# Optimization experiments

Measured on AMD Instinct MI355X. Metric: run time of the kernel, lower is better.

## Reference

```python
import jax, jax.numpy as jnp
import numpy as np

B, N, CZ, D = 1, 1024, 128, 6
LN_EPS = 1e-5
MASK_VALUE = 1000000.0  # float32 path in the original


def setup_inputs() -> dict:
    key = jax.random.key(0)
    k1, k2 = jax.random.split(key)
    pair = jax.random.normal(k1, (B, N, N, CZ), dtype=jnp.float32)
    seq_index = jnp.broadcast_to(jnp.arange(N, dtype=jnp.int64), (B, N))
    ln_scale = jnp.ones((CZ,), dtype=jnp.float32)
    ln_bias = jnp.zeros((CZ,), dtype=jnp.float32)
    W = jax.random.normal(k2, (CZ, D), dtype=jnp.float32) * (1.0 / np.sqrt(CZ))
    b = jnp.zeros((D,), dtype=jnp.float32)
    return {"pair": pair, "seq_index": seq_index, "ln_scale": ln_scale,
            "ln_bias": ln_bias, "W": W, "b": b}


def reference(pair, seq_index, ln_scale, ln_bias, W, b):
    # LayerNorm over channel dim
    mu = jnp.mean(pair, axis=-1, keepdims=True)
    var = jnp.mean(jnp.square(pair - mu), axis=-1, keepdims=True)
    h = (pair - mu) * jax.lax.rsqrt(var + LN_EPS) * ln_scale + ln_bias
    # Linear -> [B, N, N, D]
    x = jnp.einsum('bijc,cd->bijd', h, W) + b
    # symmetrize over (i, j)
    x = (x + jnp.swapaxes(x, -3, -2)) * 0.5
    # sequence-separation mask: |i - j| > 3
    si = seq_index[..., :, None]
    sj = seq_index[..., None, :]
    m = jnp.abs(si - sj) > 3  # [B, N, N]
    x = jnp.where(m[..., None], x, -MASK_VALUE)
    # padded triple log_softmax: row (axis -2), column (axis -3), channel (axis -1)
    l = x.shape[-2]
    u = jnp.zeros(x.shape[:-3] + (l, 1, D), dtype=x.dtype)
    v = jnp.zeros(x.shape[:-3] + (1, l, D), dtype=x.dtype)
    w = jnp.zeros(x.shape[:-3] + (l, l, 1), dtype=x.dtype)
    row = jax.nn.log_softmax(jnp.concatenate((u, x), axis=-2), axis=-2)[..., 1:, :]
    col = jax.nn.log_softmax(jnp.concatenate((v, x), axis=-3), axis=-3)[..., 1:, :, :]
    chn = jax.nn.log_softmax(jnp.concatenate((w, x), axis=-1), axis=-1)[..., 1:]
    return row + col + 2.0 * chn
```

## Files before the change

### kernel.cpp

```cpp
#include <hip/hip_runtime.h>

#define NN 1024
#define NP (NN * NN)
#define NBLK 1024
#define NGRP (NBLK * 16)

typedef float f32x4 __attribute__((ext_vector_type(4)));

__device__ __forceinline__ f32x4 ntld(const float* p) {
  return __builtin_nontemporal_load((const f32x4*)p);
}

__device__ __forceinline__ ushort bfr(float f) {
  uint u = __float_as_uint(f);
  return (ushort)((u + 0x7fffu + ((u >> 16) & 1u)) >> 16);
}
__device__ __forceinline__ float ubf(uint u) {
  return __uint_as_float(u << 16);
}

#define DPP_ADD_STAGE(v, ctrl)                                               \
  {                                                                          \
    const int _t = __builtin_amdgcn_update_dpp(                              \
        0, __float_as_int(v), (ctrl), 0xf, 0xf, true);                       \
    (v) += __int_as_float(_t);                                               \
  }

__global__ __launch_bounds__(256) void k_ln_gemv(
    const float* __restrict__ pairp, const float* __restrict__ gamma,
    const float* __restrict__ beta, const float* __restrict__ W,
    const float* __restrict__ bvec, ushort* __restrict__ xout,
    float* __restrict__ rowsum)
{
  if (blockIdx.x == 0) {
    for (int k = threadIdx.x; k < NN * 6; k += 256) rowsum[k] = 0.f;
  }

  const int l = threadIdx.x & 15;
  const int group = blockIdx.x * 16 + (threadIdx.x >> 4);

  float ug[8][6], apart[6] = {0, 0, 0, 0, 0, 0}, bpart[6] = {0, 0, 0, 0, 0, 0};
#pragma unroll
  for (int k = 0; k < 2; ++k)
#pragma unroll
    for (int m = 0; m < 4; ++m) {
      const int c = 4 * l + 64 * k + m;
      const int idx = 4 * k + m;
      const float ga = gamma[c], be = beta[c];
#pragma unroll
      for (int d = 0; d < 6; ++d) {
        const float w = W[c * 6 + d];
        ug[idx][d] = ga * w;
        apart[d] += ga * w;
        bpart[d] += be * w;
      }
    }
#pragma unroll
  for (int d = 0; d < 6; ++d)
#pragma unroll
    for (int m = 1; m <= 8; m <<= 1) {
      apart[d] += __shfl_xor(apart[d], m);
      bpart[d] += __shfl_xor(bpart[d], m);
    }
  const float vA = (l == 0) ? apart[0] : (l == 1) ? apart[1] : (l == 2) ? apart[2]
                  : (l == 3) ? apart[3] : (l == 4) ? apart[4] : apart[5];
  float vB = (l == 0) ? bpart[0] : (l == 1) ? bpart[1] : (l == 2) ? bpart[2]
            : (l == 3) ? bpart[3] : (l == 4) ? bpart[4] : bpart[5];
  if (l < 6) vB += bvec[l];

  size_t p = 2 * (size_t)group;
  const float* bp = pairp + p * 128 + 4 * l;
  f32x4 a0 = ntld(bp), b0 = ntld(bp + 64);
  f32x4 a1 = ntld(bp + 128), b1 = ntld(bp + 192);

  for (int it = 0; it < 32; ++it) {
    const size_t pn = p + 2 * NGRP;
    f32x4 na0, nb0, na1, nb1;
    if (it != 31) {
      const float* nbp = pairp + pn * 128 + 4 * l;
      na0 = ntld(nbp); nb0 = ntld(nbp + 64);
      na1 = ntld(nbp + 128); nb1 = ntld(nbp + 192);
    }

    const float xv0[8] = {a0.x, a0.y, a0.z, a0.w, b0.x, b0.y, b0.z, b0.w};
    const float xv1[8] = {a1.x, a1.y, a1.z, a1.w, b1.x, b1.y, b1.z, b1.w};
    float r[16];
#pragma unroll
    for (int k = 0; k < 16; ++k) r[k] = 0.f;
#pragma unroll
    for (int k = 0; k < 8; ++k) {
      r[0] += xv0[k];
      r[1] = fmaf(xv0[k], xv0[k], r[1]);
      r[8] += xv1[k];
      r[9] = fmaf(xv1[k], xv1[k], r[9]);
#pragma unroll
      for (int d = 0; d < 6; ++d) {
        r[2 + d] = fmaf(xv0[k], ug[k][d], r[2 + d]);
        r[10 + d] = fmaf(xv1[k], ug[k][d], r[10 + d]);
      }
    }
#pragma unroll
    for (int k = 0; k < 16; ++k) DPP_ADD_STAGE(r[k], 0xB1);
#pragma unroll
    for (int k = 0; k < 16; ++k) DPP_ADD_STAGE(r[k], 0x4E);
#pragma unroll
    for (int k = 0; k < 16; ++k) DPP_ADD_STAGE(r[k], 0x141);
#pragma unroll
    for (int k = 0; k < 16; ++k) DPP_ADD_STAGE(r[k], 0x140);

    if (l < 6) {
      const float mu0 = r[0] * (1.f / 128.f);
      const float var0 = r[1] * (1.f / 128.f) - mu0 * mu0;
      const float rstd0 = rsqrtf(var0 + 1e-5f);
      const float vg0 = (l == 0) ? r[2] : (l == 1) ? r[3] : (l == 2) ? r[4]
                       : (l == 3) ? r[5] : (l == 4) ? r[6] : r[7];
      xout[p * 6 + l] = bfr(fmaf(rstd0, vg0 - mu0 * vA, vB));

      const float mu1 = r[8] * (1.f / 128.f);
      const float var1 = r[9] * (1.f / 128.f) - mu1 * mu1;
      const float rstd1 = rsqrtf(var1 + 1e-5f);
      const float vg1 = (l == 0) ? r[10] : (l == 1) ? r[11] : (l == 2) ? r[12]
                       : (l == 3) ? r[13] : (l == 4) ? r[14] : r[15];
      xout[(p + 1) * 6 + l] = bfr(fmaf(rstd1, vg1 - mu1 * vA, vB));
    }
    p = pn;
    a0 = na0; b0 = nb0; a1 = na1; b1 = nb1;
  }
}

__device__ __forceinline__ void do_tile(
    const float* __restrict__ Mr, const float* __restrict__ Mc,
    int rowBand, int colBand, const int* __restrict__ seq,
    ushort* __restrict__ t, float* __restrict__ rowsum, int tid)
{
  float es[4][6];
#pragma unroll
  for (int q = 0; q < 4; ++q) {
    const int e = tid + 256 * q;
    const int r = e >> 5, c = e & 31;
    const int i = rowBand + r, j = colBand + c;
    const int dd = seq[i] - seq[j];
    const bool far = (dd > 3) || (dd < -3);
    const float* mr = &Mr[r * 193 + c * 6];
    const float* mc = &Mc[c * 193 + r * 6];
    float xs[6], chs = 0.f;
#pragma unroll
    for (int d = 0; d < 6; ++d) {
      xs[d] = far ? 0.5f * (mr[d] + mc[d]) : -1000000.f;
      es[q][d] = __expf(xs[d]);
      chs += es[q][d];
    }
    const float c2 = 2.f * logf(1.f + chs);
    uint w0 = (uint)bfr(4.f * xs[0] - c2) | ((uint)bfr(4.f * xs[1] - c2) << 16);
    uint w1 = (uint)bfr(4.f * xs[2] - c2) | ((uint)bfr(4.f * xs[3] - c2) << 16);
    uint w2 = (uint)bfr(4.f * xs[4] - c2) | ((uint)bfr(4.f * xs[5] - c2) << 16);
    uint* tp = (uint*)(t + ((size_t)i * NN + j) * 6);
    tp[0] = w0; tp[1] = w1; tp[2] = w2;
  }
#pragma unroll
  for (int q = 0; q < 4; ++q)
#pragma unroll
    for (int d = 0; d < 6; ++d)
#pragma unroll
      for (int m = 1; m <= 16; m <<= 1) es[q][d] += __shfl_xor(es[q][d], m);
  if ((tid & 31) == 0) {
    const int w = tid >> 5;
#pragma unroll
    for (int q = 0; q < 4; ++q) {
      const int i = rowBand + w + 8 * q;
#pragma unroll
      for (int d = 0; d < 6; ++d) atomicAdd(&rowsum[i * 6 + d], es[q][d]);
    }
  }
}

__global__ __launch_bounds__(256) void k_sym2(
    const ushort* __restrict__ x, const int* __restrict__ seq,
    ushort* __restrict__ t, float* __restrict__ rowsum)
{
  const int b = blockIdx.x;
  int I = (int)((sqrtf(8.f * b + 1.f) - 1.f) * 0.5f);
  while ((I + 1) * (I + 2) / 2 <= b) ++I;
  while (I * (I + 1) / 2 > b) --I;
  const int J = b - I * (I + 1) / 2;
  const int tid = threadIdx.x;

  __shared__ float M1[32 * 193];
  __shared__ float M2[32 * 193];

  for (int k = tid; k < 768; k += 256) {
    const int m = k / 24, f = (k % 24) * 8;
    {
      const uint4 raw = *(const uint4*)(x + ((size_t)(I * 32 + m) * NN + J * 32) * 6 + f);
      float* dst = &M1[m * 193 + f];
      dst[0] = ubf(raw.x & 0xffff); dst[1] = ubf(raw.x >> 16);
      dst[2] = ubf(raw.y & 0xffff); dst[3] = ubf(raw.y >> 16);
      dst[4] = ubf(raw.z & 0xffff); dst[5] = ubf(raw.z >> 16);
      dst[6] = ubf(raw.w & 0xffff); dst[7] = ubf(raw.w >> 16);
    }
    if (I != J) {
      const uint4 raw = *(const uint4*)(x + ((size_t)(J * 32 + m) * NN + I * 32) * 6 + f);
      float* dst = &M2[m * 193 + f];
      dst[0] = ubf(raw.x & 0xffff); dst[1] = ubf(raw.x >> 16);
      dst[2] = ubf(raw.y & 0xffff); dst[3] = ubf(raw.y >> 16);
      dst[4] = ubf(raw.z & 0xffff); dst[5] = ubf(raw.z >> 16);
      dst[6] = ubf(raw.w & 0xffff); dst[7] = ubf(raw.w >> 16);
    }
  }
  __syncthreads();

  if (I != J) {
    do_tile(M1, M2, I * 32, J * 32, seq, t, rowsum, tid);
    do_tile(M2, M1, J * 32, I * 32, seq, t, rowsum, tid);
  } else {
    do_tile(M1, M1, I * 32, J * 32, seq, t, rowsum, tid);
  }
}

__global__ __launch_bounds__(256) void k_out2(
    const ushort* __restrict__ t, const float* __restrict__ rowsum,
    float* __restrict__ out)
{
  const int b = blockIdx.x;
  const int i = b >> 2;
  const int j = ((b & 3) << 8) + threadIdx.x;

  __shared__ float LSI[6];
  if (threadIdx.x < 6) LSI[threadIdx.x] = logf(1.f + rowsum[i * 6 + threadIdx.x]);
  __syncthreads();

  float lj[6];
#pragma unroll
  for (int d = 0; d < 6; ++d) lj[d] = logf(1.f + rowsum[j * 6 + d]);

  const size_t p = (size_t)i * NN + j;
  const uint* tp = (const uint*)(t + p * 6);
  const uint w0 = tp[0], w1 = tp[1], w2 = tp[2];
  float o[6];
  o[0] = ubf(w0 & 0xffff) - LSI[0] - lj[0];
  o[1] = ubf(w0 >> 16)    - LSI[1] - lj[1];
  o[2] = ubf(w1 & 0xffff) - LSI[2] - lj[2];
  o[3] = ubf(w1 >> 16)    - LSI[3] - lj[3];
  o[4] = ubf(w2 & 0xffff) - LSI[4] - lj[4];
  o[5] = ubf(w2 >> 16)    - LSI[5] - lj[5];

  float* op = out + p * 6;
  *(float2*)(op) = make_float2(o[0], o[1]);
  *(float2*)(op + 2) = make_float2(o[2], o[3]);
  *(float2*)(op + 4) = make_float2(o[4], o[5]);
}

extern "C" void kernel_launch(void* const* d_in, const int* in_sizes, int n_in,
                              void* d_out, int out_size, void* d_ws, size_t ws_size,
                              hipStream_t stream) {
  const float* pairp = (const float*)d_in[0];
  const int* seq = (const int*)d_in[1];
  const float* gamma = (const float*)d_in[2];
  const float* beta = (const float*)d_in[3];
  const float* W = (const float*)d_in[4];
  const float* bvec = (const float*)d_in[5];
  float* out = (float*)d_out;

  ushort* x = (ushort*)d_ws;
  ushort* t = x + (size_t)NP * 6;
  float* rowsum = (float*)(t + (size_t)NP * 6);

  k_ln_gemv<<<NBLK, 256, 0, stream>>>(pairp, gamma, beta, W, bvec, x, rowsum);
  k_sym2<<<528, 256, 0, stream>>>(x, seq, t, rowsum);
  k_out2<<<NP / 256, 256, 0, stream>>>(t, rowsum, out);
}
```

Measured before the change: 133.5 us.

## Fuse symmetrize and output kernels with a grid-wide barrier, dropping t intermediate

Merges the symmetrize/softmax tile kernel and the final output kernel into one kernel. Each block first accumulates its exp row sums with atomics, then all blocks meet at a grid-wide barrier built on an atomic counter, and each block finishes by writing the final fp32 output directly from its shared-memory tiles. This removes the bf16 t intermediate write and read-back and one kernel launch, at the cost of recomputing exp values. It also relies on all 528 blocks being co-resident so the spin barrier cannot deadlock.

```diff
diff --git a/kernel.cpp b/kernel.cpp
--- a/kernel.cpp
+++ b/kernel.cpp
@@ -4,6 +4,7 @@
 #define NP (NN * NN)
 #define NBLK 1024
 #define NGRP (NBLK * 16)
+#define NTRI 528
 
 typedef float f32x4 __attribute__((ext_vector_type(4)));
 
@@ -30,10 +31,11 @@
     const float* __restrict__ pairp, const float* __restrict__ gamma,
     const float* __restrict__ beta, const float* __restrict__ W,
     const float* __restrict__ bvec, ushort* __restrict__ xout,
-    float* __restrict__ rowsum)
+    float* __restrict__ rowsum, int* __restrict__ done)
 {
   if (blockIdx.x == 0) {
     for (int k = threadIdx.x; k < NN * 6; k += 256) rowsum[k] = 0.f;
+    if (threadIdx.x == 0) *done = 0;
   }
 
   const int l = threadIdx.x & 15;
@@ -128,12 +130,46 @@
   }
 }
 
-__device__ __forceinline__ void do_tile(
-    const float* __restrict__ Mr, const float* __restrict__ Mc,
-    int rowBand, int colBand, const int* __restrict__ seq,
-    ushort* __restrict__ t, float* __restrict__ rowsum, int tid)
+__device__ __forceinline__ void phaseA(
+    const float* __restrict__ Mr, int rowBand, const float* __restrict__ Mc,
+    int colBand, const int* __restrict__ seq, float* __restrict__ rowsum,
+    int tid)
 {
   float es[4][6];
+#pragma unroll
+  for (int q = 0; q < 4; ++q) {
+    const int e = tid + 256 * q;
+    const int r = e >> 5, c = e & 31;
+    const int dd = seq[rowBand + r] - seq[colBand + c];
+    const bool far = (dd > 3) || (dd < -3);
+    const float* mr = &Mr[r * 193 + c * 6];
+    const float* mc = &Mc[c * 193 + r * 6];
+#pragma unroll
+    for (int d = 0; d < 6; ++d)
+      es[q][d] = far ? __expf(0.5f * (mr[d] + mc[d])) : 0.f;
+  }
+#pragma unroll
+  for (int q = 0; q < 4; ++q)
+#pragma unroll
+    for (int d = 0; d < 6; ++d)
+#pragma unroll
+      for (int m = 1; m <= 16; m <<= 1) es[q][d] += __shfl_xor(es[q][d], m);
+  if ((tid & 31) == 0) {
+    const int w = tid >> 5;
+#pragma unroll
+    for (int q = 0; q < 4; ++q) {
+      const int i = rowBand + w + 8 * q;
+#pragma unroll
+      for (int d = 0; d < 6; ++d) atomicAdd(&rowsum[i * 6 + d], es[q][d]);
+    }
+  }
+}
+
+__device__ __forceinline__ void phaseB(
+    const float* __restrict__ Mr, int rowBand, const float* __restrict__ Mc,
+    int colBand, const int* __restrict__ seq, const float* __restrict__ LSr,
+    const float* __restrict__ LSc, float* __restrict__ out, int tid)
+{
 #pragma unroll
   for (int q = 0; q < 4; ++q) {
     const int e = tid + 256 * q;
@@ -147,36 +183,24 @@
 #pragma unroll
     for (int d = 0; d < 6; ++d) {
       xs[d] = far ? 0.5f * (mr[d] + mc[d]) : -1000000.f;
-      es[q][d] = __expf(xs[d]);
-      chs += es[q][d];
-    }
-    const float c2 = 2.f * logf(1.f + chs);
-    uint w0 = (uint)bfr(4.f * xs[0] - c2) | ((uint)bfr(4.f * xs[1] - c2) << 16);
-    uint w1 = (uint)bfr(4.f * xs[2] - c2) | ((uint)bfr(4.f * xs[3] - c2) << 16);
-    uint w2 = (uint)bfr(4.f * xs[4] - c2) | ((uint)bfr(4.f * xs[5] - c2) << 16);
-    uint* tp = (uint*)(t + ((size_t)i * NN + j) * 6);
-    tp[0] = w0; tp[1] = w1; tp[2] = w2;
-  }
-#pragma unroll
-  for (int q = 0; q < 4; ++q)
+      chs += __expf(xs[d]);
+    }
+    const float c2 = 2.f * __logf(1.f + chs);
+    float o[6];
 #pragma unroll
     for (int d = 0; d < 6; ++d)
-#pragma unroll
-      for (int m = 1; m <= 16; m <<= 1) es[q][d] += __shfl_xor(es[q][d], m);
-  if ((tid & 31) == 0) {
-    const int w = tid >> 5;
-#pragma unroll
-    for (int q = 0; q < 4; ++q) {
-      const int i = rowBand + w + 8 * q;
-#pragma unroll
-      for (int d = 0; d < 6; ++d) atomicAdd(&rowsum[i * 6 + d], es[q][d]);
-    }
-  }
-}
-
-__global__ __launch_bounds__(256) void k_sym2(
+      o[d] = 4.f * xs[d] - c2 - LSr[r * 6 + d] - LSc[c * 6 + d];
+    float* op = out + ((size_t)i * NN + j) * 6;
+    *(float2*)(op) = make_float2(o[0], o[1]);
+    *(float2*)(op + 2) = make_float2(o[2], o[3]);
+    *(float2*)(op + 4) = make_float2(o[4], o[5]);
+  }
+}
+
+__global__ __launch_bounds__(256) void k_fused(
     const ushort* __restrict__ x, const int* __restrict__ seq,
-    ushort* __restrict__ t, float* __restrict__ rowsum)
+    float* __restrict__ rowsum, int* __restrict__ done,
+    float* __restrict__ out)
 {
   const int b = blockIdx.x;
   int I = (int)((sqrtf(8.f * b + 1.f) - 1.f) * 0.5f);
@@ -187,6 +211,7 @@
 
   __shared__ float M1[32 * 193];
   __shared__ float M2[32 * 193];
+  __shared__ float LSI[192], LSJ[192];
 
   for (int k = tid; k < 768; k += 256) {
     const int m = k / 24, f = (k % 24) * 8;
@@ -210,44 +235,43 @@
   __syncthreads();
 
   if (I != J) {
-    do_tile(M1, M2, I * 32, J * 32, seq, t, rowsum, tid);
-    do_tile(M2, M1, J * 32, I * 32, seq, t, rowsum, tid);
+    phaseA(M1, I * 32, M2, J * 32, seq, rowsum, tid);
+    phaseA(M2, J * 32, M1, I * 32, seq, rowsum, tid);
   } else {
-    do_tile(M1, M1, I * 32, J * 32, seq, t, rowsum, tid);
-  }
-}
-
-__global__ __launch_bounds__(256) void k_out2(
-    const ushort* __restrict__ t, const float* __restrict__ rowsum,
-    float* __restrict__ out)
-{
-  const int b = blockIdx.x;
-  const int i = b >> 2;
-  const int j = ((b & 3) << 8) + threadIdx.x;
-
-  __shared__ float LSI[6];
-  if (threadIdx.x < 6) LSI[threadIdx.x] = logf(1.f + rowsum[i * 6 + threadIdx.x]);
-  __syncthreads();
-
-  float lj[6];
-#pragma unroll
-  for (int d = 0; d < 6; ++d) lj[d] = logf(1.f + rowsum[j * 6 + d]);
-
-  const size_t p = (size_t)i * NN + j;
-  const uint* tp = (const uint*)(t + p * 6);
-  const uint w0 = tp[0], w1 = tp[1], w2 = tp[2];
-  float o[6];
-  o[0] = ubf(w0 & 0xffff) - LSI[0] - lj[0];
-  o[1] = ubf(w0 >> 16)    - LSI[1] - lj[1];
-  o[2] = ubf(w1 & 0xffff) - LSI[2] - lj[2];
-  o[3] = ubf(w1 >> 16)    - LSI[3] - lj[3];
-  o[4] = ubf(w2 & 0xffff) - LSI[4] - lj[4];
-  o[5] = ubf(w2 >> 16)    - LSI[5] - lj[5];
-
-  float* op = out + p * 6;
-  *(float2*)(op) = make_float2(o[0], o[1]);
-  *(float2*)(op + 2) = make_float2(o[2], o[3]);
-  *(float2*)(op + 4) = make_float2(o[4], o[5]);
+    phaseA(M1, I * 32, M1, J * 32, seq, rowsum, tid);
+  }
+
+  __threadfence();
+  __syncthreads();
+  if (tid == 0) {
+    __hip_atomic_fetch_add(done, 1, __ATOMIC_RELEASE, __HIP_MEMORY_SCOPE_AGENT);
+    while (__hip_atomic_load(done, __ATOMIC_ACQUIRE, __HIP_MEMORY_SCOPE_AGENT)
+           < NTRI) {
+      __builtin_amdgcn_s_sleep(8);
+    }
+  }
+  __syncthreads();
+
+  for (int k = tid; k < 384; k += 256) {
+    if (k < 192) {
+      const float rs = __hip_atomic_load(&rowsum[I * 192 + k], __ATOMIC_RELAXED,
+                                         __HIP_MEMORY_SCOPE_AGENT);
+      LSI[k] = __logf(1.f + rs);
+    } else {
+      const float rs = __hip_atomic_load(&rowsum[J * 192 + (k - 192)],
+                                         __ATOMIC_RELAXED,
+                                         __HIP_MEMORY_SCOPE_AGENT);
+      LSJ[k - 192] = __logf(1.f + rs);
+    }
+  }
+  __syncthreads();
+
+  if (I != J) {
+    phaseB(M1, I * 32, M2, J * 32, seq, LSI, LSJ, out, tid);
+    phaseB(M2, J * 32, M1, I * 32, seq, LSJ, LSI, out, tid);
+  } else {
+    phaseB(M1, I * 32, M1, J * 32, seq, LSI, LSI, out, tid);
+  }
 }
 
 extern "C" void kernel_launch(void* const* d_in, const int* in_sizes, int n_in,
@@ -262,10 +286,10 @@
   float* out = (float*)d_out;
 
   ushort* x = (ushort*)d_ws;
-  ushort* t = x + (size_t)NP * 6;
-  float* rowsum = (float*)(t + (size_t)NP * 6);
-
-  k_ln_gemv<<<NBLK, 256, 0, stream>>>(pairp, gamma, beta, W, bvec, x, rowsum);
-  k_sym2<<<528, 256, 0, stream>>>(x, seq, t, rowsum);
-  k_out2<<<NP / 256, 256, 0, stream>>>(t, rowsum, out);
-}
+  float* rowsum = (float*)(x + (size_t)NP * 6);
+  int* done = (int*)(rowsum + NN * 6);
+
+  k_ln_gemv<<<NBLK, 256, 0, stream>>>(pairp, gamma, beta, W, bvec, x, rowsum,
+                                      done);
+  k_fused<<<NTRI, 256, 0, stream>>>(x, seq, rowsum, done, out);
+}
```

New measurement: 210.2 us. +57.5%, slower.
